# Optimization experiments

Measured on AMD Instinct MI355X. Metric: run time of the kernel, lower is better.

Reference implementation:

```python
import jax, jax.numpy as jnp
import numpy as np
import math

N, T, D, H = 64, 512, 512, 512

def setup_inputs() -> dict:
    key = jax.random.key(0)
    k1, k2, k3, k4 = jax.random.split(key, 4)
    x = jax.random.normal(k1, (N, T, D), dtype=jnp.float32)
    h0 = jax.random.normal(k2, (N, H), dtype=jnp.float32)
    Wx = jax.random.normal(k3, (D, 4 * H), dtype=jnp.float32) / math.sqrt(D)
    Wh = jax.random.normal(k4, (H, 4 * H), dtype=jnp.float32) / math.sqrt(H)
    b = jnp.zeros((4 * H,), dtype=jnp.float32)
    return {"x": x, "h0": h0, "Wx": Wx, "Wh": Wh, "b": b}

def reference(x, h0, Wx, Wh, b):
    # Precompute input projections for all timesteps as one big GEMM: [N,T,4H]
    xW = jnp.einsum('ntd,dk->ntk', x, Wx) + b
    c0 = jnp.zeros_like(h0)

    def step(carry, xw_t):
        h, c = carry
        gates = xw_t + h @ Wh          # [N,4H]
        i, f, o, g = jnp.split(gates, 4, axis=1)
        i = jax.nn.sigmoid(i)
        f = jax.nn.sigmoid(f)
        o = jax.nn.sigmoid(o)
        g = jnp.tanh(g)
        c = f * c + i * g
        h = o * jnp.tanh(c)
        return (h, c), h

    # scan over time: move T to leading axis
    (_, _), hs = jax.lax.scan(step, (h0, c0), jnp.swapaxes(xW, 0, 1))
    return jnp.swapaxes(hs, 0, 1)  # [N,T,H]
```

## Files before the change

kernel.cpp:

```cpp
#include <hip/hip_runtime.h>
#include <cstddef>


typedef _Float16 half8 __attribute__((ext_vector_type(8)));
typedef float f32x4 __attribute__((ext_vector_type(4)));
typedef unsigned u32x4 __attribute__((ext_vector_type(4)));

#define NBATCH 64
#define TSTEPS 512
#define DIN    512
#define HID    512
#define NCOL   2048
#define SCAN_WGS 128
#define HSLOT  (NBATCH * HID)

__device__ __forceinline__ float fast_sigmoid(float x) {
  return 1.0f / (1.0f + __expf(-x));
}
__device__ __forceinline__ float fast_tanh(float x) {
  return 1.0f - 2.0f / (__expf(2.0f * x) + 1.0f);
}

__global__ void lstm_prep(const float* __restrict__ x, const float* __restrict__ h0,
                          _Float16* __restrict__ xb, _Float16* __restrict__ hbuf,
                          unsigned* __restrict__ flags)
{
  size_t gid = (size_t)blockIdx.x * blockDim.x + threadIdx.x;
  size_t stride = (size_t)gridDim.x * blockDim.x;
  const size_t NX = (size_t)NBATCH * TSTEPS * DIN;
  for (size_t i = gid * 4; i < NX; i += stride * 4) {
    float4 v = *(const float4*)(x + i);
    xb[i + 0] = (_Float16)v.x;
    xb[i + 1] = (_Float16)v.y;
    xb[i + 2] = (_Float16)v.z;
    xb[i + 3] = (_Float16)v.w;
  }
  for (size_t i = gid; i < (size_t)HSLOT; i += stride)
    hbuf[i] = (_Float16)h0[i];
  if (gid < SCAN_WGS) flags[gid] = 0u;
}

__global__ __launch_bounds__(256, 1) void lstm_scan(
    const _Float16* __restrict__ xb,
    const float* __restrict__ Wx,
    const float* __restrict__ Wh,
    const float* __restrict__ bias,
    _Float16* __restrict__ hbuf,
    float* __restrict__ out,
    unsigned* __restrict__ flags)
{
  __shared__ half8 WxF[16][64];
  __shared__ half8 WhF[16][64];

  const int wg   = blockIdx.x;
  const int tid  = threadIdx.x;
  const int lane = tid & 63;
  const int wave = tid >> 6;

  {
    const int gate = tid & 3;
    const int k0   = tid >> 2;
    _Float16* wx = (_Float16*)WxF;
    _Float16* wh = (_Float16*)WhF;
    for (int pass = 0; pass < 8; ++pass) {
      int k = k0 + pass * 64;
      float4 vx = *(const float4*)(Wx + (size_t)k * NCOL + gate * 512 + wg * 4);
      float4 vh = *(const float4*)(Wh + (size_t)k * NCOL + gate * 512 + wg * 4);
      int base = (k >> 5) * 512 + (((k >> 3) & 3) * 16 + gate * 4) * 8 + (k & 7);
      wx[base + 0 * 8] = (_Float16)vx.x;
      wx[base + 1 * 8] = (_Float16)vx.y;
      wx[base + 2 * 8] = (_Float16)vx.z;
      wx[base + 3 * 8] = (_Float16)vx.w;
      wh[base + 0 * 8] = (_Float16)vh.x;
      wh[base + 1 * 8] = (_Float16)vh.y;
      wh[base + 2 * 8] = (_Float16)vh.z;
      wh[base + 3 * 8] = (_Float16)vh.w;
    }
  }
  __syncthreads();

  const int fr = lane & 15;
  const int q  = lane >> 4;
  const int fk = q * 8;
  const int mrow = wave * 16 + fr;

  const float bias_fr = bias[(fr >> 2) * 512 + wg * 4 + (fr & 3)];

  const int jw   = fr >> 2;
  const int nw   = wave * 16 + q * 4 + jw;
  const int colw = wg * 4 + (fr & 3);

  float c0 = 0.f, c1 = 0.f, c2 = 0.f, c3 = 0.f;

  half8 xa[16];
#pragma unroll
  for (int ks = 0; ks < 16; ++ks)
    xa[ks] = *(const half8*)(xb + ((size_t)mrow * TSTEPS + 0) * DIN + ks * 32 + fk);

  const unsigned long long* flag64 = (const unsigned long long*)flags;

  for (int t = 0; t < TSTEPS; ++t) {
    if (t) {
      if (tid < 64) {
        for (;;) {
          unsigned long long v = __hip_atomic_load(
              flag64 + tid, __ATOMIC_RELAXED, __HIP_MEMORY_SCOPE_AGENT);
          bool pok = ((unsigned)v >= (unsigned)t) &&
                     ((unsigned)(v >> 32) >= (unsigned)t);
          if (__all(pok)) break;
          __builtin_amdgcn_s_sleep(2);
        }
      }
      __syncthreads();
    }

    f32x4 a0 = {0.f, 0.f, 0.f, 0.f};
    f32x4 a1 = {0.f, 0.f, 0.f, 0.f};
    f32x4 a2 = {0.f, 0.f, 0.f, 0.f};
    f32x4 a3 = {0.f, 0.f, 0.f, 0.f};
#pragma unroll
    for (int ks = 0; ks < 16; ks += 4) {
      a0 = __builtin_amdgcn_mfma_f32_16x16x32_f16(xa[ks],     WxF[ks][lane],     a0, 0, 0, 0);
      a1 = __builtin_amdgcn_mfma_f32_16x16x32_f16(xa[ks + 1], WxF[ks + 1][lane], a1, 0, 0, 0);
      a2 = __builtin_amdgcn_mfma_f32_16x16x32_f16(xa[ks + 2], WxF[ks + 2][lane], a2, 0, 0, 0);
      a3 = __builtin_amdgcn_mfma_f32_16x16x32_f16(xa[ks + 3], WxF[ks + 3][lane], a3, 0, 0, 0);
    }

    {
      const _Float16* hbase = hbuf + (size_t)(t & 1) * HSLOT +
                              (size_t)mrow * HID + q * 8;
      u32x4 v0, v1, v2, v3, v4, v5, v6, v7, v8, v9, va, vb, vc, vd, ve, vf;
      asm volatile(
        "global_load_dwordx4 %0, %16, off sc1\n\t"
        "global_load_dwordx4 %1, %16, off offset:64 sc1\n\t"
        "global_load_dwordx4 %2, %16, off offset:128 sc1\n\t"
        "global_load_dwordx4 %3, %16, off offset:192 sc1\n\t"
        "global_load_dwordx4 %4, %16, off offset:256 sc1\n\t"
        "global_load_dwordx4 %5, %16, off offset:320 sc1\n\t"
        "global_load_dwordx4 %6, %16, off offset:384 sc1\n\t"
        "global_load_dwordx4 %7, %16, off offset:448 sc1\n\t"
        "global_load_dwordx4 %8, %16, off offset:512 sc1\n\t"
        "global_load_dwordx4 %9, %16, off offset:576 sc1\n\t"
        "global_load_dwordx4 %10, %16, off offset:640 sc1\n\t"
        "global_load_dwordx4 %11, %16, off offset:704 sc1\n\t"
        "global_load_dwordx4 %12, %16, off offset:768 sc1\n\t"
        "global_load_dwordx4 %13, %16, off offset:832 sc1\n\t"
        "global_load_dwordx4 %14, %16, off offset:896 sc1\n\t"
        "global_load_dwordx4 %15, %16, off offset:960 sc1\n\t"
        "s_waitcnt vmcnt(0)"
        : "=&v"(v0), "=&v"(v1), "=&v"(v2), "=&v"(v3),
          "=&v"(v4), "=&v"(v5), "=&v"(v6), "=&v"(v7),
          "=&v"(v8), "=&v"(v9), "=&v"(va), "=&v"(vb),
          "=&v"(vc), "=&v"(vd), "=&v"(ve), "=&v"(vf)
        : "v"(hbase)
        : "memory");

#define HMFMA(KS, ACC, V) \
      ACC = __builtin_amdgcn_mfma_f32_16x16x32_f16( \
          __builtin_bit_cast(half8, V), WhF[KS][lane], ACC, 0, 0, 0);
      HMFMA(0,  a0, v0) HMFMA(1,  a1, v1) HMFMA(2,  a2, v2) HMFMA(3,  a3, v3)
      HMFMA(4,  a0, v4) HMFMA(5,  a1, v5) HMFMA(6,  a2, v6) HMFMA(7,  a3, v7)
      HMFMA(8,  a0, v8) HMFMA(9,  a1, v9) HMFMA(10, a2, va) HMFMA(11, a3, vb)
      HMFMA(12, a0, vc) HMFMA(13, a1, vd) HMFMA(14, a2, ve) HMFMA(15, a3, vf)
#undef HMFMA
    }
    f32x4 acc = (a0 + a1) + (a2 + a3);

    float h0v, h1v, h2v, h3v;
#define LSTM_CELL(J, CJ, HJ)                                                  \
    {                                                                         \
      float av = acc[J] + bias_fr;                                            \
      float v4 = __shfl_xor(av, 4);                                           \
      float alo = (fr & 4) ? v4 : av;                                         \
      float ahi = (fr & 4) ? av : v4;                                         \
      float blo = __shfl_xor(alo, 8);                                         \
      float bhi = __shfl_xor(ahi, 8);                                         \
      float iv = (fr & 8) ? blo : alo;                         \
      float fv = (fr & 8) ? bhi : ahi;                         \
      float ov = (fr & 8) ? alo : blo;                         \
      float gv = (fr & 8) ? ahi : bhi;                         \
      float ig = fast_sigmoid(iv);                                            \
      float fg = fast_sigmoid(fv);                                            \
      float og = fast_sigmoid(ov);                                            \
      float gg = fast_tanh(gv);                                               \
      CJ = fg * CJ + ig * gg;                                                 \
      HJ = og * fast_tanh(CJ);                                                \
    }
    LSTM_CELL(0, c0, h0v)
    LSTM_CELL(1, c1, h1v)
    LSTM_CELL(2, c2, h2v)
    LSTM_CELL(3, c3, h3v)
#undef LSTM_CELL

    float hsel = (jw == 0) ? h0v : (jw == 1) ? h1v : (jw == 2) ? h2v : h3v;

    {
      float hpart = __shfl_xor(hsel, 1);
      if ((fr & 1) == 0) {
        _Float16 lo = (_Float16)hsel, hi = (_Float16)hpart;
        unsigned packed = (unsigned)__builtin_bit_cast(unsigned short, lo) |
                          ((unsigned)__builtin_bit_cast(unsigned short, hi) << 16);
        unsigned* hdst = (unsigned*)(hbuf + (size_t)((t + 1) & 1) * HSLOT +
                                     (size_t)nw * HID + colw);
        __hip_atomic_store(hdst, packed, __ATOMIC_RELAXED, __HIP_MEMORY_SCOPE_AGENT);
      }
    }
    out[((size_t)nw * TSTEPS + t) * HID + colw] = hsel;

    asm volatile("s_waitcnt vmcnt(0)" ::: "memory");
    __syncthreads();
    if (tid == 0)
      __hip_atomic_store(&flags[wg], (unsigned)(t + 1),
                         __ATOMIC_RELAXED, __HIP_MEMORY_SCOPE_AGENT);

    if (t + 1 < TSTEPS) {
#pragma unroll
      for (int ks = 0; ks < 16; ++ks)
        xa[ks] = *(const half8*)(xb + ((size_t)mrow * TSTEPS + (t + 1)) * DIN + ks * 32 + fk);
    }
  }
}

extern "C" void kernel_launch(void* const* d_in, const int* in_sizes, int n_in,
                              void* d_out, int out_size, void* d_ws, size_t ws_size,
                              hipStream_t stream) {
  const float* x  = (const float*)d_in[0];
  const float* h0 = (const float*)d_in[1];
  const float* Wx = (const float*)d_in[2];
  const float* Wh = (const float*)d_in[3];
  const float* b  = (const float*)d_in[4];
  float* out = (float*)d_out;

  char* ws = (char*)d_ws;
  _Float16* xb    = (_Float16*)ws;
  _Float16* hbuf  = (_Float16*)(ws + 33554432);
  unsigned* flags = (unsigned*)(ws + 33554432 + 262144);

  lstm_prep<<<dim3(2048), dim3(256), 0, stream>>>(x, h0, xb, hbuf, flags);
  lstm_scan<<<dim3(SCAN_WGS), dim3(256), 0, stream>>>(xb, Wx, Wh, b, hbuf, out, flags);
}
```

Baseline: 3.009 ms.

## Pad barrier flags per cache line, overlap h loads with Wx MFMAs, widen h stores

Each workgroup's progress flag now sits in its own 128-byte slot, so flag stores from different workgroups stop contending on shared cache lines. Pollers read two padded flags per lane and spin with a shorter sleep. The recurrent h loads are issued before the input-projection MFMAs and waited on only afterwards, hiding global latency behind compute. The h writes are packed into one 64-bit atomic store per four columns instead of two 32-bit stores. The workspace must hold the larger flag array (128*32 words), which is not checked here.

```diff
diff --git a/kernel.cpp b/kernel.cpp
--- a/kernel.cpp
+++ b/kernel.cpp
@@ -13,6 +13,7 @@
 #define NCOL   2048
 #define SCAN_WGS 128
 #define HSLOT  (NBATCH * HID)
+#define FPAD   32
 
 __device__ __forceinline__ float fast_sigmoid(float x) {
   return 1.0f / (1.0f + __expf(-x));
@@ -37,7 +38,7 @@
   }
   for (size_t i = gid; i < (size_t)HSLOT; i += stride)
     hbuf[i] = (_Float16)h0[i];
-  if (gid < SCAN_WGS) flags[gid] = 0u;
+  if (gid < SCAN_WGS * FPAD) flags[gid] = 0u;
 }
 
 __global__ __launch_bounds__(256, 1) void lstm_scan(
@@ -97,39 +98,26 @@
   for (int ks = 0; ks < 16; ++ks)
     xa[ks] = *(const half8*)(xb + ((size_t)mrow * TSTEPS + 0) * DIN + ks * 32 + fk);
 
-  const unsigned long long* flag64 = (const unsigned long long*)flags;
-
   for (int t = 0; t < TSTEPS; ++t) {
     if (t) {
       if (tid < 64) {
+        const unsigned* f0 = flags + (size_t)lane * FPAD;
+        const unsigned* f1 = flags + (size_t)(lane + 64) * FPAD;
         for (;;) {
-          unsigned long long v = __hip_atomic_load(
-              flag64 + tid, __ATOMIC_RELAXED, __HIP_MEMORY_SCOPE_AGENT);
-          bool pok = ((unsigned)v >= (unsigned)t) &&
-                     ((unsigned)(v >> 32) >= (unsigned)t);
+          unsigned a = __hip_atomic_load(f0, __ATOMIC_RELAXED, __HIP_MEMORY_SCOPE_AGENT);
+          unsigned b = __hip_atomic_load(f1, __ATOMIC_RELAXED, __HIP_MEMORY_SCOPE_AGENT);
+          bool pok = (a >= (unsigned)t) && (b >= (unsigned)t);
           if (__all(pok)) break;
-          __builtin_amdgcn_s_sleep(2);
+          __builtin_amdgcn_s_sleep(1);
         }
       }
       __syncthreads();
     }
 
-    f32x4 a0 = {0.f, 0.f, 0.f, 0.f};
-    f32x4 a1 = {0.f, 0.f, 0.f, 0.f};
-    f32x4 a2 = {0.f, 0.f, 0.f, 0.f};
-    f32x4 a3 = {0.f, 0.f, 0.f, 0.f};
-#pragma unroll
-    for (int ks = 0; ks < 16; ks += 4) {
-      a0 = __builtin_amdgcn_mfma_f32_16x16x32_f16(xa[ks],     WxF[ks][lane],     a0, 0, 0, 0);
-      a1 = __builtin_amdgcn_mfma_f32_16x16x32_f16(xa[ks + 1], WxF[ks + 1][lane], a1, 0, 0, 0);
-      a2 = __builtin_amdgcn_mfma_f32_16x16x32_f16(xa[ks + 2], WxF[ks + 2][lane], a2, 0, 0, 0);
-      a3 = __builtin_amdgcn_mfma_f32_16x16x32_f16(xa[ks + 3], WxF[ks + 3][lane], a3, 0, 0, 0);
-    }
-
+    u32x4 v0, v1, v2, v3, v4, v5, v6, v7, v8, v9, va, vb, vc, vd, ve, vf;
     {
       const _Float16* hbase = hbuf + (size_t)(t & 1) * HSLOT +
                               (size_t)mrow * HID + q * 8;
-      u32x4 v0, v1, v2, v3, v4, v5, v6, v7, v8, v9, va, vb, vc, vd, ve, vf;
       asm volatile(
         "global_load_dwordx4 %0, %16, off sc1\n\t"
         "global_load_dwordx4 %1, %16, off offset:64 sc1\n\t"
@@ -146,24 +134,43 @@
         "global_load_dwordx4 %12, %16, off offset:768 sc1\n\t"
         "global_load_dwordx4 %13, %16, off offset:832 sc1\n\t"
         "global_load_dwordx4 %14, %16, off offset:896 sc1\n\t"
-        "global_load_dwordx4 %15, %16, off offset:960 sc1\n\t"
-        "s_waitcnt vmcnt(0)"
+        "global_load_dwordx4 %15, %16, off offset:960 sc1"
         : "=&v"(v0), "=&v"(v1), "=&v"(v2), "=&v"(v3),
           "=&v"(v4), "=&v"(v5), "=&v"(v6), "=&v"(v7),
           "=&v"(v8), "=&v"(v9), "=&v"(va), "=&v"(vb),
           "=&v"(vc), "=&v"(vd), "=&v"(ve), "=&v"(vf)
         : "v"(hbase)
         : "memory");
+    }
+
+    f32x4 a0 = {0.f, 0.f, 0.f, 0.f};
+    f32x4 a1 = {0.f, 0.f, 0.f, 0.f};
+    f32x4 a2 = {0.f, 0.f, 0.f, 0.f};
+    f32x4 a3 = {0.f, 0.f, 0.f, 0.f};
+#pragma unroll
+    for (int ks = 0; ks < 16; ks += 4) {
+      a0 = __builtin_amdgcn_mfma_f32_16x16x32_f16(xa[ks],     WxF[ks][lane],     a0, 0, 0, 0);
+      a1 = __builtin_amdgcn_mfma_f32_16x16x32_f16(xa[ks + 1], WxF[ks + 1][lane], a1, 0, 0, 0);
+      a2 = __builtin_amdgcn_mfma_f32_16x16x32_f16(xa[ks + 2], WxF[ks + 2][lane], a2, 0, 0, 0);
+      a3 = __builtin_amdgcn_mfma_f32_16x16x32_f16(xa[ks + 3], WxF[ks + 3][lane], a3, 0, 0, 0);
+    }
+
+    asm volatile("s_waitcnt vmcnt(0)"
+        : "+v"(v0), "+v"(v1), "+v"(v2), "+v"(v3),
+          "+v"(v4), "+v"(v5), "+v"(v6), "+v"(v7),
+          "+v"(v8), "+v"(v9), "+v"(va), "+v"(vb),
+          "+v"(vc), "+v"(vd), "+v"(ve), "+v"(vf)
+        :: "memory");
+    __builtin_amdgcn_sched_barrier(0);
 
 #define HMFMA(KS, ACC, V) \
-      ACC = __builtin_amdgcn_mfma_f32_16x16x32_f16( \
-          __builtin_bit_cast(half8, V), WhF[KS][lane], ACC, 0, 0, 0);
-      HMFMA(0,  a0, v0) HMFMA(1,  a1, v1) HMFMA(2,  a2, v2) HMFMA(3,  a3, v3)
-      HMFMA(4,  a0, v4) HMFMA(5,  a1, v5) HMFMA(6,  a2, v6) HMFMA(7,  a3, v7)
-      HMFMA(8,  a0, v8) HMFMA(9,  a1, v9) HMFMA(10, a2, va) HMFMA(11, a3, vb)
-      HMFMA(12, a0, vc) HMFMA(13, a1, vd) HMFMA(14, a2, ve) HMFMA(15, a3, vf)
+    ACC = __builtin_amdgcn_mfma_f32_16x16x32_f16( \
+        __builtin_bit_cast(half8, V), WhF[KS][lane], ACC, 0, 0, 0);
+    HMFMA(0,  a0, v0) HMFMA(1,  a1, v1) HMFMA(2,  a2, v2) HMFMA(3,  a3, v3)
+    HMFMA(4,  a0, v4) HMFMA(5,  a1, v5) HMFMA(6,  a2, v6) HMFMA(7,  a3, v7)
+    HMFMA(8,  a0, v8) HMFMA(9,  a1, v9) HMFMA(10, a2, va) HMFMA(11, a3, vb)
+    HMFMA(12, a0, vc) HMFMA(13, a1, vd) HMFMA(14, a2, ve) HMFMA(15, a3, vf)
 #undef HMFMA
-    }
     f32x4 acc = (a0 + a1) + (a2 + a3);
 
     float h0v, h1v, h2v, h3v;
@@ -195,14 +202,18 @@
     float hsel = (jw == 0) ? h0v : (jw == 1) ? h1v : (jw == 2) ? h2v : h3v;
 
     {
-      float hpart = __shfl_xor(hsel, 1);
-      if ((fr & 1) == 0) {
-        _Float16 lo = (_Float16)hsel, hi = (_Float16)hpart;
-        unsigned packed = (unsigned)__builtin_bit_cast(unsigned short, lo) |
-                          ((unsigned)__builtin_bit_cast(unsigned short, hi) << 16);
-        unsigned* hdst = (unsigned*)(hbuf + (size_t)((t + 1) & 1) * HSLOT +
-                                     (size_t)nw * HID + colw);
-        __hip_atomic_store(hdst, packed, __ATOMIC_RELAXED, __HIP_MEMORY_SCOPE_AGENT);
+      float hp1 = __shfl_xor(hsel, 1);
+      _Float16 e0 = (_Float16)hsel, e1 = (_Float16)hp1;
+      unsigned pair = (unsigned)__builtin_bit_cast(unsigned short, e0) |
+                      ((unsigned)__builtin_bit_cast(unsigned short, e1) << 16);
+      unsigned other = __builtin_bit_cast(unsigned,
+          __shfl_xor(__builtin_bit_cast(float, pair), 2));
+      if ((fr & 3) == 0) {
+        unsigned long long w = (unsigned long long)pair |
+                               ((unsigned long long)other << 32);
+        unsigned long long* hdst = (unsigned long long*)
+            (hbuf + (size_t)((t + 1) & 1) * HSLOT + (size_t)nw * HID + wg * 4);
+        __hip_atomic_store(hdst, w, __ATOMIC_RELAXED, __HIP_MEMORY_SCOPE_AGENT);
       }
     }
     out[((size_t)nw * TSTEPS + t) * HID + colw] = hsel;
@@ -210,7 +221,7 @@
     asm volatile("s_waitcnt vmcnt(0)" ::: "memory");
     __syncthreads();
     if (tid == 0)
-      __hip_atomic_store(&flags[wg], (unsigned)(t + 1),
+      __hip_atomic_store(&flags[(size_t)wg * FPAD], (unsigned)(t + 1),
                          __ATOMIC_RELAXED, __HIP_MEMORY_SCOPE_AGENT);
 
     if (t + 1 < TSTEPS) {
```

After: 2.952 ms. Within noise of the previous version (-1.9%).
